# Performance work log

Measured on AMD Instinct MI355X. Metric: run time of the kernel, lower is better.

The kernel has to match this reference:

```python
import jax, jax.numpy as jnp
import numpy as np

NEG_SLOPE = 0.2
LN_EPS = 1e-5
NUM_LAYERS = 4
H = 3            # num heads (both modalities)
C_MOL = 512      # molecule channels (in == out, required by the cat in forward)
C_PROT = 1280    # protein channels
VOCAB = 512 * 9 + 1
G_MOL = 512      # molecule graphs
G_PROT = 32      # protein graphs


def _with_self_loops(src, dst, n):
    loop = jnp.arange(n, dtype=src.dtype)
    return jnp.concatenate([src, loop]), jnp.concatenate([dst, loop])


def gat_conv(x, src, dst, W, a_src, a_dst, bias):
    """PyG GATConv, concat=False (head-mean), add_self_loops=True.
    x: [N, Fin], W: [Fin, H*C], a_src/a_dst: [H, C], bias: [C]."""
    n = x.shape[0]
    h = (x @ W).reshape(n, a_src.shape[0], a_src.shape[1])   # [N,H,C]
    al_s = jnp.sum(h * a_src, axis=-1)                       # [N,H]
    al_d = jnp.sum(h * a_dst, axis=-1)                       # [N,H]
    s, d = _with_self_loops(src, dst, n)
    e = jax.nn.leaky_relu(al_s[s] + al_d[d], NEG_SLOPE)      # [E+N,H]
    m = jax.ops.segment_max(e, d, num_segments=n)            # segment softmax (stable)
    m = jnp.where(jnp.isfinite(m), m, 0.0)
    p = jnp.exp(e - m[d])
    z = jax.ops.segment_sum(p, d, num_segments=n)
    alpha = p / (z[d] + 1e-16)                               # [E+N,H]
    out = jax.ops.segment_sum(h[s] * alpha[:, :, None], d, num_segments=n)  # [N,H,C]
    return out.mean(axis=1) + bias                           # concat=False -> head mean


def layer_norm(x, g, b):
    mu = x.mean(-1, keepdims=True)
    var = ((x - mu) ** 2).mean(-1, keepdims=True)
    return (x - mu) * jax.lax.rsqrt(var + LN_EPS) * g + b


def mean_pool(x, batch, num_graphs):
    s = jax.ops.segment_sum(x, batch, num_segments=num_graphs)
    cnt = jax.ops.segment_sum(jnp.ones((x.shape[0],), x.dtype), batch, num_segments=num_graphs)
    return s / jnp.maximum(cnt, 1.0)[:, None]


def setup_inputs() -> dict:
    key = jax.random.key(0)
    ks = jax.random.split(key, 20)
    n_mol, e_mol = 40000, 80000
    n_prot, e_prot = 8000, 64000
    drug_x = jax.random.randint(ks[0], (n_mol, 9), 0, VOCAB)
    mol_edge_index = jax.random.randint(ks[1], (2, e_mol), 0, n_mol)
    mol_batch = jnp.sort(jax.random.randint(ks[2], (n_mol,), 0, G_MOL))
    prot_x = jax.random.normal(ks[3], (n_prot, C_PROT), jnp.float32)
    prot_edge_index = jax.random.randint(ks[4], (2, e_prot), 0, n_prot)
    prot_batch = jnp.sort(jax.random.randint(ks[5], (n_prot,), 0, G_PROT))
    sc = 0.02
    emb = (jax.random.normal(ks[6], (VOCAB, C_MOL), jnp.float32) * sc).at[0].set(0.0)  # padding_idx=0
    mol_W = jax.random.normal(ks[7], (NUM_LAYERS, C_MOL, H * C_MOL), jnp.float32) * sc
    mol_asrc = jax.random.normal(ks[8], (NUM_LAYERS, H, C_MOL), jnp.float32) * sc
    mol_adst = jax.random.normal(ks[9], (NUM_LAYERS, H, C_MOL), jnp.float32) * sc
    mol_bias = jnp.zeros((NUM_LAYERS, C_MOL), jnp.float32)
    mol_ln_g = jnp.ones((NUM_LAYERS, C_MOL), jnp.float32)
    mol_ln_b = jnp.zeros((NUM_LAYERS, C_MOL), jnp.float32)
    prot_W = jax.random.normal(ks[10], (NUM_LAYERS, C_PROT, H * C_PROT), jnp.float32) * sc
    prot_asrc = jax.random.normal(ks[11], (NUM_LAYERS, H, C_PROT), jnp.float32) * sc
    prot_adst = jax.random.normal(ks[12], (NUM_LAYERS, H, C_PROT), jnp.float32) * sc
    prot_bias = jnp.zeros((NUM_LAYERS, C_PROT), jnp.float32)
    prot_ln_g = jnp.ones((NUM_LAYERS, C_PROT), jnp.float32)
    prot_ln_b = jnp.zeros((NUM_LAYERS, C_PROT), jnp.float32)
    return dict(drug_x=drug_x, mol_edge_index=mol_edge_index, mol_batch=mol_batch,
                prot_x=prot_x, prot_edge_index=prot_edge_index, prot_batch=prot_batch,
                emb=emb, mol_W=mol_W, mol_asrc=mol_asrc, mol_adst=mol_adst,
                mol_bias=mol_bias, mol_ln_g=mol_ln_g, mol_ln_b=mol_ln_b,
                prot_W=prot_W, prot_asrc=prot_asrc, prot_adst=prot_adst,
                prot_bias=prot_bias, prot_ln_g=prot_ln_g, prot_ln_b=prot_ln_b)


def reference(drug_x, mol_edge_index, mol_batch, prot_x, prot_edge_index, prot_batch,
              emb, mol_W, mol_asrc, mol_adst, mol_bias, mol_ln_g, mol_ln_b,
              prot_W, prot_asrc, prot_adst, prot_bias, prot_ln_g, prot_ln_b):
    # dropout layers are identity (eval mode)
    mol_x = emb[drug_x].mean(axis=-2)                       # [N_mol, C_MOL]
    mol_feats = [mean_pool(mol_x, mol_batch, G_MOL)]
    prot_feats = [mean_pool(prot_x, prot_batch, G_PROT)]
    msrc, mdst = mol_edge_index[0], mol_edge_index[1]
    psrc, pdst = prot_edge_index[0], prot_edge_index[1]
    px = prot_x
    for i in range(NUM_LAYERS):
        mol_x = gat_conv(mol_x, msrc, mdst, mol_W[i], mol_asrc[i], mol_adst[i], mol_bias[i])
        mol_x = layer_norm(mol_x, mol_ln_g[i], mol_ln_b[i])
        px = gat_conv(px, psrc, pdst, prot_W[i], prot_asrc[i], prot_adst[i], prot_bias[i])
        px = layer_norm(px, prot_ln_g[i], prot_ln_b[i])
        mol_feats.append(mean_pool(mol_x, mol_batch, G_MOL))
        prot_feats.append(mean_pool(px, prot_batch, G_PROT))
    return jnp.stack(mol_feats, axis=1), jnp.stack(prot_feats, axis=1)  # [G,5,C] each
```

## Files before the change

kernel.cpp:

```cpp
#include <hip/hip_runtime.h>
#include <cstdint>


constexpr int H_HEADS = 3;
constexpr float NEG_SLOPE = 0.2f;
constexpr float LN_EPS = 1e-5f;
constexpr int N_MOL = 40000, E_MOL = 80000, C_MOL = 512, G_MOL = 512;
constexpr int N_PROT = 8000, E_PROT = 64000, C_PROT = 1280, G_PROT = 32;
constexpr int LAYERS = 4;
constexpr int MPAD_MOL = 40064;
constexpr int MPAD_PROT = 8064;

typedef unsigned short u16;
typedef __attribute__((ext_vector_type(8))) short short8v;
typedef __attribute__((ext_vector_type(4))) unsigned short ushort4v;
typedef __attribute__((ext_vector_type(4))) float f32x4;

__device__ __forceinline__ float bf2f(u16 s) {
    union { unsigned u; float f; } v; v.u = ((unsigned)s) << 16; return v.f;
}
__device__ __forceinline__ u16 f2bf(float f) {
    union { float f; unsigned u; } v; v.f = f;
    return (u16)((v.u + 0x7fffu + ((v.u >> 16) & 1u)) >> 16);
}

__device__ __forceinline__ void g2l16(const void* g, void* l) {
    __builtin_amdgcn_global_load_lds((const __attribute__((address_space(1))) void*)g,
                                     (__attribute__((address_space(3))) void*)l, 16, 0, 0);
}


__global__ void set_int_kernel(int* p, int v, int n) {
    int i = blockIdx.x * blockDim.x + threadIdx.x;
    if (i < n) p[i] = v;
}

__global__ void zero_f32_kernel(float* p, int n) {
    int i = blockIdx.x * blockDim.x + threadIdx.x;
    if (i < n) p[i] = 0.f;
}

__global__ void copy_int_kernel(const int* __restrict__ s, int* __restrict__ d, int n) {
    int i = blockIdx.x * blockDim.x + threadIdx.x;
    if (i < n) d[i] = s[i];
}

__global__ void hist_kernel(const int* __restrict__ keys, int n, int* __restrict__ cnt) {
    int i = blockIdx.x * blockDim.x + threadIdx.x;
    if (i < n) atomicAdd(&cnt[keys[i]], 1);
}

__global__ void scan_kernel(const int* __restrict__ in, int* __restrict__ out, int n) {
    __shared__ int sums[1024];
    const int t = threadIdx.x;
    const int chunk = (n + 1023) / 1024;
    const int start = t * chunk;
    const int end = min(start + chunk, n);
    int s = 0;
    for (int i = start; i < end; ++i) s += in[i];
    sums[t] = s;
    __syncthreads();
    if (t == 0) {
        int acc = 0;
        for (int i = 0; i < 1024; ++i) { int v = sums[i]; sums[i] = acc; acc += v; }
        out[n] = acc;
    }
    __syncthreads();
    int acc = sums[t];
    for (int i = start; i < end; ++i) { out[i] = acc; acc += in[i]; }
}

__global__ void fill_self_kernel(int* __restrict__ pos, int* __restrict__ srcl, int n) {
    int i = blockIdx.x * blockDim.x + threadIdx.x;
    if (i < n) { int slot = atomicAdd(&pos[i], 1); srcl[slot] = i; }
}

__global__ void fill_edge_kernel(const int* __restrict__ src, const int* __restrict__ dst, int e,
                                 int* __restrict__ pos, int* __restrict__ srcl) {
    int i = blockIdx.x * blockDim.x + threadIdx.x;
    if (i < e) { int slot = atomicAdd(&pos[dst[i]], 1); srcl[slot] = src[i]; }
}

__global__ void f32_to_bf16(const float* __restrict__ in, u16* __restrict__ out, int n) {
    int i = blockIdx.x * blockDim.x + threadIdx.x;
    if (i < n) out[i] = f2bf(in[i]);
}


__global__ void embed_mean_kernel(const int* __restrict__ drug_x, const float* __restrict__ emb,
                                  u16* __restrict__ out) {
    const int n = blockIdx.x;
    __shared__ int idx[9];
    if (threadIdx.x < 9) idx[threadIdx.x] = drug_x[n * 9 + threadIdx.x];
    __syncthreads();
    const int c = threadIdx.x;
    float s = 0.f;
#pragma unroll
    for (int t = 0; t < 9; ++t) s += emb[(size_t)idx[t] * C_MOL + c];
    out[(size_t)n * C_MOL + c] = f2bf(s * (1.f / 9.f));
}


__global__ __launch_bounds__(256) void transfold(const float* __restrict__ W, u16* __restrict__ Wt,
                                                 const float* __restrict__ asrc,
                                                 const float* __restrict__ adst,
                                                 float* __restrict__ wsrc, float* __restrict__ wdst,
                                                 int CIN, int COUT, size_t headStride, int ldn) {
    __shared__ float t[32][33];
    __shared__ float rs[8][33], rd[8][33];
    const int h = blockIdx.z;
    const int n0 = blockIdx.x * 32, k0 = blockIdx.y * 32;
    const int tx = threadIdx.x & 31, ty = threadIdx.x >> 5;
#pragma unroll
    for (int q = 0; q < 4; ++q)
        t[ty + q * 8][tx] = W[(size_t)(k0 + ty + q * 8) * (H_HEADS * COUT) + h * COUT + n0 + tx];
    __syncthreads();
#pragma unroll
    for (int q = 0; q < 4; ++q)
        Wt[(size_t)h * headStride + (size_t)(n0 + ty + q * 8) * ldn + k0 + tx] =
            f2bf(t[tx][ty + q * 8]);
    float ps = 0.f, pd = 0.f;
    const float* as = asrc + h * COUT + n0;
    const float* ad = adst + h * COUT + n0;
#pragma unroll
    for (int q = 0; q < 4; ++q) {
        const float w = t[tx][ty + q * 8];
        ps += w * as[ty + q * 8];
        pd += w * ad[ty + q * 8];
    }
    rs[ty][tx] = ps;
    rd[ty][tx] = pd;
    __syncthreads();
    if (ty == 0) {
        float s = 0.f, d = 0.f;
#pragma unroll
        for (int j = 0; j < 8; ++j) { s += rs[j][tx]; d += rd[j][tx]; }
        atomicAdd(&wsrc[h * CIN + k0 + tx], s);
        atomicAdd(&wdst[h * CIN + k0 + tx], d);
    }
}


template <int C>
__global__ void attn_logits(const u16* __restrict__ x, const float* __restrict__ wsrc,
                            const float* __restrict__ wdst, float* __restrict__ als,
                            float* __restrict__ ald) {
    constexpr int PER = C / 64;
    const int n = blockIdx.x, lane = threadIdx.x;
    const u16* xr = x + (size_t)n * C + lane * PER;
    float xv[PER];
#pragma unroll
    for (int i = 0; i < PER; i += 4) {
        const ushort4v v = *(const ushort4v*)(xr + i);
        xv[i] = bf2f(v.x); xv[i + 1] = bf2f(v.y); xv[i + 2] = bf2f(v.z); xv[i + 3] = bf2f(v.w);
    }
    for (int h = 0; h < H_HEADS; ++h) {
        const float* ws = wsrc + h * C + lane * PER;
        const float* wd = wdst + h * C + lane * PER;
        float ss = 0.f, sd = 0.f;
#pragma unroll
        for (int i = 0; i < PER; i += 4) {
            const float4 a = *(const float4*)(ws + i);
            const float4 b = *(const float4*)(wd + i);
            ss += xv[i] * a.x + xv[i + 1] * a.y + xv[i + 2] * a.z + xv[i + 3] * a.w;
            sd += xv[i] * b.x + xv[i + 1] * b.y + xv[i + 2] * b.z + xv[i + 3] * b.w;
        }
        for (int o = 32; o; o >>= 1) { ss += __shfl_down(ss, o); sd += __shfl_down(sd, o); }
        if (lane == 0) { als[n * H_HEADS + h] = ss; ald[n * H_HEADS + h] = sd; }
    }
}


__global__ __launch_bounds__(256) void agg_mol_f(const u16* __restrict__ x,
                                                 const float* __restrict__ als,
                                                 const float* __restrict__ ald,
                                                 const int* __restrict__ indptr,
                                                 const int* __restrict__ srcl,
                                                 u16* __restrict__ agg) {
    constexpr int MAXD = 128;
    const int wv = threadIdx.x >> 6, lane = threadIdx.x & 63;
    const int n = blockIdx.x * 4 + wv;
    const int beg = indptr[n], end = indptr[n + 1];
    const int deg = end - beg;
    __shared__ float atab[4][MAXD * 3];
    float m = -1e30f, zi = 0.f;
    if (lane < H_HEADS) {
        const float ad = ald[n * H_HEADS + lane];
        for (int e = beg; e < end; ++e) {
            float v = als[srcl[e] * H_HEADS + lane] + ad;
            v = v >= 0.f ? v : NEG_SLOPE * v;
            m = fmaxf(m, v);
        }
        float z = 0.f;
        for (int e = beg; e < end; ++e) {
            float v = als[srcl[e] * H_HEADS + lane] + ad;
            v = v >= 0.f ? v : NEG_SLOPE * v;
            z += __expf(v - m);
        }
        zi = 1.f / (z + 1e-16f);
    }
    const float m0 = __shfl(m, 0), m1 = __shfl(m, 1), m2 = __shfl(m, 2);
    const float z0 = __shfl(zi, 0), z1 = __shfl(zi, 1), z2 = __shfl(zi, 2);
    const float ad0 = ald[n * H_HEADS + 0], ad1 = ald[n * H_HEADS + 1], ad2 = ald[n * H_HEADS + 2];
    const bool fits = deg <= MAXD;
    if (fits) {
        for (int i = lane; i < deg * 3; i += 64) {
            const int e = i / 3, h = i - e * 3;
            float v = als[srcl[beg + e] * H_HEADS + h] + (h == 0 ? ad0 : (h == 1 ? ad1 : ad2));
            v = v >= 0.f ? v : NEG_SLOPE * v;
            const float mh = h == 0 ? m0 : (h == 1 ? m1 : m2);
            const float zh = h == 0 ? z0 : (h == 1 ? z1 : z2);
            atab[wv][i] = __expf(v - mh) * zh;
        }
    }
    __syncthreads();
    float acc[H_HEADS][8];
#pragma unroll
    for (int h = 0; h < H_HEADS; ++h)
#pragma unroll
        for (int j = 0; j < 8; ++j) acc[h][j] = 0.f;
    for (int e = 0; e < deg; ++e) {
        const int s = srcl[beg + e];
        float a0, a1, a2;
        if (fits) {
            a0 = atab[wv][e * 3 + 0];
            a1 = atab[wv][e * 3 + 1];
            a2 = atab[wv][e * 3 + 2];
        } else {
            float v0 = als[s * H_HEADS + 0] + ad0; v0 = v0 >= 0.f ? v0 : NEG_SLOPE * v0;
            float v1 = als[s * H_HEADS + 1] + ad1; v1 = v1 >= 0.f ? v1 : NEG_SLOPE * v1;
            float v2 = als[s * H_HEADS + 2] + ad2; v2 = v2 >= 0.f ? v2 : NEG_SLOPE * v2;
            a0 = __expf(v0 - m0) * z0;
            a1 = __expf(v1 - m1) * z1;
            a2 = __expf(v2 - m2) * z2;
        }
        const short8v row = *(const short8v*)(x + (size_t)s * C_MOL + lane * 8);
#pragma unroll
        for (int j = 0; j < 8; ++j) {
            const float f = bf2f((u16)row[j]);
            acc[0][j] += a0 * f; acc[1][j] += a1 * f; acc[2][j] += a2 * f;
        }
    }
    u16* o = agg + (size_t)n * (3 * C_MOL) + lane * 8;
#pragma unroll
    for (int h = 0; h < H_HEADS; ++h) {
        short8v r;
#pragma unroll
        for (int j = 0; j < 8; ++j) r[j] = (short)f2bf(acc[h][j]);
        *(short8v*)(o + h * C_MOL) = r;
    }
}


__global__ __launch_bounds__(320) void agg_prot_f(const u16* __restrict__ x,
                                                  const float* __restrict__ als,
                                                  const float* __restrict__ ald,
                                                  const int* __restrict__ indptr,
                                                  const int* __restrict__ srcl,
                                                  u16* __restrict__ agg) {
    constexpr int MAXD = 512;
    const int n = blockIdx.x, tid = threadIdx.x;
    const int beg = indptr[n], end = indptr[n + 1];
    const int deg = end - beg;
    __shared__ float mz[6];
    __shared__ float atab[MAXD * 3];
    if (tid < H_HEADS) {
        const float ad = ald[n * H_HEADS + tid];
        float m = -1e30f;
        for (int e = beg; e < end; ++e) {
            float v = als[srcl[e] * H_HEADS + tid] + ad;
            v = v >= 0.f ? v : NEG_SLOPE * v;
            m = fmaxf(m, v);
        }
        float z = 0.f;
        for (int e = beg; e < end; ++e) {
            float v = als[srcl[e] * H_HEADS + tid] + ad;
            v = v >= 0.f ? v : NEG_SLOPE * v;
            z += __expf(v - m);
        }
        mz[tid] = m;
        mz[3 + tid] = 1.f / (z + 1e-16f);
    }
    __syncthreads();
    const bool fits = deg <= MAXD;
    if (fits) {
        for (int i = tid; i < deg * 3; i += 320) {
            const int e = i / 3, h = i - e * 3;
            float v = als[srcl[beg + e] * H_HEADS + h] + ald[n * H_HEADS + h];
            v = v >= 0.f ? v : NEG_SLOPE * v;
            atab[i] = __expf(v - mz[h]) * mz[3 + h];
        }
    }
    __syncthreads();
    const float m0 = mz[0], m1 = mz[1], m2 = mz[2];
    const float z0 = mz[3], z1 = mz[4], z2 = mz[5];
    const float ad0 = ald[n * H_HEADS + 0], ad1 = ald[n * H_HEADS + 1], ad2 = ald[n * H_HEADS + 2];
    float acc[H_HEADS][4];
#pragma unroll
    for (int h = 0; h < H_HEADS; ++h)
#pragma unroll
        for (int j = 0; j < 4; ++j) acc[h][j] = 0.f;
    for (int e = 0; e < deg; ++e) {
        const int s = srcl[beg + e];
        float a0, a1, a2;
        if (fits) {
            a0 = atab[e * 3 + 0];
            a1 = atab[e * 3 + 1];
            a2 = atab[e * 3 + 2];
        } else {
            float v0 = als[s * H_HEADS + 0] + ad0; v0 = v0 >= 0.f ? v0 : NEG_SLOPE * v0;
            float v1 = als[s * H_HEADS + 1] + ad1; v1 = v1 >= 0.f ? v1 : NEG_SLOPE * v1;
            float v2 = als[s * H_HEADS + 2] + ad2; v2 = v2 >= 0.f ? v2 : NEG_SLOPE * v2;
            a0 = __expf(v0 - m0) * z0;
            a1 = __expf(v1 - m1) * z1;
            a2 = __expf(v2 - m2) * z2;
        }
        const ushort4v v = *(const ushort4v*)(x + (size_t)s * C_PROT + tid * 4);
        const float f0 = bf2f(v.x), f1 = bf2f(v.y), f2 = bf2f(v.z), f3 = bf2f(v.w);
        acc[0][0] += a0 * f0; acc[0][1] += a0 * f1; acc[0][2] += a0 * f2; acc[0][3] += a0 * f3;
        acc[1][0] += a1 * f0; acc[1][1] += a1 * f1; acc[1][2] += a1 * f2; acc[1][3] += a1 * f3;
        acc[2][0] += a2 * f0; acc[2][1] += a2 * f1; acc[2][2] += a2 * f2; acc[2][3] += a2 * f3;
    }
    u16* o = agg + (size_t)n * (3 * C_PROT) + tid * 4;
#pragma unroll
    for (int h = 0; h < H_HEADS; ++h) {
        ushort4v r;
        r.x = f2bf(acc[h][0]); r.y = f2bf(acc[h][1]); r.z = f2bf(acc[h][2]); r.w = f2bf(acc[h][3]);
        *(ushort4v*)(o + h * C_PROT) = r;
    }
}


__global__ __launch_bounds__(256) void gemm128d(
    const u16* __restrict__ A0, const u16* __restrict__ B0, u16* __restrict__ C0,
    int N0, int K0, int nx0, int M0, int g0,
    const u16* __restrict__ A1, const u16* __restrict__ B1, u16* __restrict__ C1,
    int N1, int K1, int nx1, int M1) {
    __shared__ u16 lds[16384];
    const int tid = threadIdx.x;
    const int w = tid >> 6, l = tid & 63;
    const int wr = w >> 1, wc = w & 1;

    const int bid = blockIdx.x;
    const u16 *A, *Bt;
    u16* Cout;
    int N, K, nxch, Mreal, base, sz;
    if (bid < g0) { base = 0; sz = g0; A = A0; Bt = B0; Cout = C0; N = N0; K = K0; nxch = nx0; Mreal = M0; }
    else { base = g0; sz = gridDim.x - g0; A = A1; Bt = B1; Cout = C1; N = N1; K = K1; nxch = nx1; Mreal = M1; }
    const int j = bid - base;
    const int q = sz >> 3, r = sz & 7;
    const int xcd = j & 7, idx = j >> 3;
    const int wg = (xcd < r ? xcd * (q + 1) : r * (q + 1) + (xcd - r) * q) + idx;
    const int nx = wg % nxch, my = wg / nxch;
    const size_t bm = (size_t)my * 128, bn = (size_t)nx * 128;

    const f32x4 zf = {0.f, 0.f, 0.f, 0.f};
    f32x4 acc[4][4];
#pragma unroll
    for (int i = 0; i < 4; ++i)
#pragma unroll
        for (int jj = 0; jj < 4; ++jj) acc[i][jj] = zf;

    const int srow = w * 32 + (l >> 3);
    const int sseg = (l & 7) ^ (l >> 3);
    const u16* Ab = A + (bm + srow) * (size_t)K + sseg * 8;
    const u16* Bb = Bt + (bn + srow) * (size_t)K + sseg * 8;

    for (int k0 = 0; k0 < K; k0 += 64) {
#pragma unroll
        for (int qq = 0; qq < 4; ++qq)
            g2l16(Ab + k0 + (size_t)qq * 8 * K, lds + (w * 4 + qq) * 512);
#pragma unroll
        for (int qq = 0; qq < 4; ++qq)
            g2l16(Bb + k0 + (size_t)qq * 8 * K, lds + 8192 + (w * 4 + qq) * 512);
        __syncthreads();
#pragma unroll
        for (int kk = 0; kk < 2; ++kk) {
            const int sg = ((kk * 4 + (l >> 4)) ^ (l & 7)) * 8;
            short8v af[4], bf8[4];
#pragma unroll
            for (int fm = 0; fm < 4; ++fm) {
                const int row = wr * 64 + fm * 16 + (l & 15);
                af[fm] = *(const short8v*)&lds[row * 64 + sg];
            }
#pragma unroll
            for (int fn = 0; fn < 4; ++fn) {
                const int row = wc * 64 + fn * 16 + (l & 15);
                bf8[fn] = *(const short8v*)&lds[8192 + row * 64 + sg];
            }
#pragma unroll
            for (int fm = 0; fm < 4; ++fm)
#pragma unroll
                for (int fn = 0; fn < 4; ++fn)
                    acc[fm][fn] = __builtin_amdgcn_mfma_f32_16x16x32_bf16(af[fm], bf8[fn],
                                                                          acc[fm][fn], 0, 0, 0);
        }
        __syncthreads();
    }

#pragma unroll
    for (int half = 0; half < 2; ++half) {
        if (wr == half) {
#pragma unroll
            for (int fm = 0; fm < 4; ++fm)
#pragma unroll
                for (int fn = 0; fn < 4; ++fn) {
                    const int col = wc * 64 + fn * 16 + (l & 15);
#pragma unroll
                    for (int rr = 0; rr < 4; ++rr)
                        lds[(fm * 16 + (l >> 4) * 4 + rr) * 136 + col] = f2bf(acc[fm][fn][rr]);
                }
        }
        __syncthreads();
        const int lrow = tid >> 2, lseg = tid & 3;
        const size_t grow = bm + half * 64 + lrow;
        if (grow < (size_t)Mreal) {
            u16* Crow = Cout + grow * (size_t)N + bn + lseg * 32;
            const u16* Lr = lds + lrow * 136 + lseg * 32;
#pragma unroll
            for (int ii = 0; ii < 4; ++ii)
                *(float4*)(Crow + ii * 8) = *(const float4*)(Lr + ii * 8);
        }
        __syncthreads();
    }
}


template <int C, int LOGITS>
__global__ __launch_bounds__(C / 4) void ln_kernel(u16* __restrict__ x,
                                                   const float* __restrict__ bias,
                                                   const float* __restrict__ g,
                                                   const float* __restrict__ b,
                                                   const float* __restrict__ wsrc_n,
                                                   const float* __restrict__ wdst_n,
                                                   float* __restrict__ als,
                                                   float* __restrict__ ald) {
    constexpr int NT = C / 4;
    constexpr int NW = NT / 64;
    const int n = blockIdx.x, tid = threadIdx.x;
    u16* xr = x + (size_t)n * C + tid * 4;
    constexpr float invH = 1.f / (float)H_HEADS;
    const ushort4v xv = *(const ushort4v*)xr;
    const float4 bi = *(const float4*)(bias + tid * 4);
    const float v0 = bf2f(xv.x) * invH + bi.x;
    const float v1 = bf2f(xv.y) * invH + bi.y;
    const float v2 = bf2f(xv.z) * invH + bi.z;
    const float v3 = bf2f(xv.w) * invH + bi.w;
    float s1 = v0 + v1 + v2 + v3;
    float s2 = v0 * v0 + v1 * v1 + v2 * v2 + v3 * v3;
    __shared__ float red[2][NW];
    __shared__ float red2[NW][6];
    for (int o = 32; o; o >>= 1) { s1 += __shfl_down(s1, o); s2 += __shfl_down(s2, o); }
    if ((tid & 63) == 0) { red[0][tid >> 6] = s1; red[1][tid >> 6] = s2; }
    __syncthreads();
    float t1 = 0.f, t2 = 0.f;
#pragma unroll
    for (int i = 0; i < NW; ++i) { t1 += red[0][i]; t2 += red[1][i]; }
    const float mu = t1 / C;
    const float var = t2 / C - mu * mu;
    const float rstd = rsqrtf(var + LN_EPS);
    const float4 gg = *(const float4*)(g + tid * 4);
    const float4 bb = *(const float4*)(b + tid * 4);
    ushort4v ov;
    ov.x = f2bf((v0 - mu) * rstd * gg.x + bb.x);
    ov.y = f2bf((v1 - mu) * rstd * gg.y + bb.y);
    ov.z = f2bf((v2 - mu) * rstd * gg.z + bb.z);
    ov.w = f2bf((v3 - mu) * rstd * gg.w + bb.w);
    *(ushort4v*)xr = ov;
    if (LOGITS) {
        const float q0 = bf2f(ov.x), q1 = bf2f(ov.y), q2 = bf2f(ov.z), q3 = bf2f(ov.w);
        float ps[3], pd[3];
#pragma unroll
        for (int h = 0; h < 3; ++h) {
            const float4 a = *(const float4*)(wsrc_n + h * C + tid * 4);
            const float4 d = *(const float4*)(wdst_n + h * C + tid * 4);
            ps[h] = q0 * a.x + q1 * a.y + q2 * a.z + q3 * a.w;
            pd[h] = q0 * d.x + q1 * d.y + q2 * d.z + q3 * d.w;
        }
        for (int o = 32; o; o >>= 1) {
#pragma unroll
            for (int h = 0; h < 3; ++h) {
                ps[h] += __shfl_down(ps[h], o);
                pd[h] += __shfl_down(pd[h], o);
            }
        }
        if ((tid & 63) == 0) {
            const int wv = tid >> 6;
#pragma unroll
            for (int h = 0; h < 3; ++h) { red2[wv][h] = ps[h]; red2[wv][3 + h] = pd[h]; }
        }
        __syncthreads();
        if (tid == 0) {
#pragma unroll
            for (int h = 0; h < 3; ++h) {
                float as = 0.f, ad = 0.f;
#pragma unroll
                for (int i = 0; i < NW; ++i) { as += red2[i][h]; ad += red2[i][3 + h]; }
                als[n * H_HEADS + h] = as;
                ald[n * H_HEADS + h] = ad;
            }
        }
    }
}


template <int C, int S>
__global__ void pool_atomic(const u16* __restrict__ x, const int* __restrict__ goff,
                            float* __restrict__ out, int layer) {
    const int g = blockIdx.x, seg = blockIdx.y;
    const int beg = goff[g], end = goff[g + 1];
    const int len = end - beg;
    const int s0 = beg + (len * seg) / S;
    const int s1 = beg + (len * (seg + 1)) / S;
    if (s0 >= s1) return;
    const float inv = 1.f / fmaxf((float)len, 1.f);
    const int tid = threadIdx.x;
    float a0 = 0.f, a1 = 0.f, a2 = 0.f, a3 = 0.f;
    for (int n = s0; n < s1; ++n) {
        const ushort4v v = *(const ushort4v*)(x + (size_t)n * C + tid * 4);
        a0 += bf2f(v.x); a1 += bf2f(v.y); a2 += bf2f(v.z); a3 += bf2f(v.w);
    }
    float* o = out + ((size_t)g * (LAYERS + 1) + layer) * C + tid * 4;
    atomicAdd(o + 0, a0 * inv);
    atomicAdd(o + 1, a1 * inv);
    atomicAdd(o + 2, a2 * inv);
    atomicAdd(o + 3, a3 * inv);
}


extern "C" void kernel_launch(void* const* d_in, const int* in_sizes, int n_in, void* d_out,
                              int out_size, void* d_ws, size_t ws_size, hipStream_t stream) {
    const int* drug_x      = (const int*)d_in[0];
    const int* mol_ei      = (const int*)d_in[1];
    const int* mol_batch   = (const int*)d_in[2];
    const float* prot_in   = (const float*)d_in[3];
    const int* prot_ei     = (const int*)d_in[4];
    const int* prot_batch  = (const int*)d_in[5];
    const float* emb       = (const float*)d_in[6];
    const float* mol_W     = (const float*)d_in[7];
    const float* mol_asrc  = (const float*)d_in[8];
    const float* mol_adst  = (const float*)d_in[9];
    const float* mol_bias  = (const float*)d_in[10];
    const float* mol_lng   = (const float*)d_in[11];
    const float* mol_lnb   = (const float*)d_in[12];
    const float* prot_W    = (const float*)d_in[13];
    const float* prot_asrc = (const float*)d_in[14];
    const float* prot_adst = (const float*)d_in[15];
    const float* prot_bias = (const float*)d_in[16];
    const float* prot_lng  = (const float*)d_in[17];
    const float* prot_lnb  = (const float*)d_in[18];

    if (ws_size < (size_t)240500000) return;
    const bool BIG = ws_size >= (size_t)262000000;

    char* base = (char*)d_ws;
    size_t off = 0;
    auto alloc = [&](size_t bytes) -> void* {
        void* r = base + off;
        off = (off + bytes + 255) & ~(size_t)255;
        return r;
    };
    u16* x_mol  = (u16*)alloc((size_t)N_MOL * C_MOL * 2);
    u16* x_prot = (u16*)alloc((size_t)N_PROT * C_PROT * 2);
    u16* aggM   = (u16*)alloc((size_t)3 * MPAD_MOL * C_MOL * 2);
    u16* WtM    = (u16*)alloc((size_t)H_HEADS * C_MOL * C_MOL * 2);
    u16* WtP    = (u16*)alloc((size_t)H_HEADS * C_PROT * C_PROT * 2);
    u16* aggP   = BIG ? (u16*)alloc((size_t)3 * MPAD_PROT * C_PROT * 2) : aggM;
    float* wsrcM = (float*)alloc((size_t)LAYERS * H_HEADS * C_MOL * 4);
    float* wdstM = (float*)alloc((size_t)LAYERS * H_HEADS * C_MOL * 4);
    float* wsrcP = (float*)alloc((size_t)LAYERS * H_HEADS * C_PROT * 4);
    float* wdstP = (float*)alloc((size_t)LAYERS * H_HEADS * C_PROT * 4);
    float* alsM = (float*)alloc((size_t)N_MOL * H_HEADS * 4);
    float* aldM = (float*)alloc((size_t)N_MOL * H_HEADS * 4);
    float* alsP = (float*)alloc((size_t)N_PROT * H_HEADS * 4);
    float* aldP = (float*)alloc((size_t)N_PROT * H_HEADS * 4);
    int* mol_indptr  = (int*)alloc((N_MOL + 1) * 4);
    int* mol_pos     = (int*)alloc(N_MOL * 4);
    int* mol_srcl    = (int*)alloc((E_MOL + N_MOL) * 4);
    int* prot_indptr = (int*)alloc((N_PROT + 1) * 4);
    int* prot_pos    = (int*)alloc(N_PROT * 4);
    int* prot_srcl   = (int*)alloc((E_PROT + N_PROT) * 4);
    int* cnt         = (int*)alloc(N_MOL * 4);
    int* mol_goff    = (int*)alloc((G_MOL + 1) * 4);
    int* prot_goff   = (int*)alloc((G_PROT + 1) * 4);
    int* gcnt        = (int*)alloc(G_MOL * 4);

    float* out_mol  = (float*)d_out;
    float* out_prot = (float*)d_out + (size_t)G_MOL * (LAYERS + 1) * C_MOL;

    zero_f32_kernel<<<(out_size + 255) / 256, 256, 0, stream>>>((float*)d_out, out_size);
    zero_f32_kernel<<<(LAYERS * H_HEADS * C_MOL + 255) / 256, 256, 0, stream>>>(
        wsrcM, LAYERS * H_HEADS * C_MOL);
    zero_f32_kernel<<<(LAYERS * H_HEADS * C_MOL + 255) / 256, 256, 0, stream>>>(
        wdstM, LAYERS * H_HEADS * C_MOL);
    zero_f32_kernel<<<(LAYERS * H_HEADS * C_PROT + 255) / 256, 256, 0, stream>>>(
        wsrcP, LAYERS * H_HEADS * C_PROT);
    zero_f32_kernel<<<(LAYERS * H_HEADS * C_PROT + 255) / 256, 256, 0, stream>>>(
        wdstP, LAYERS * H_HEADS * C_PROT);

    set_int_kernel<<<(N_MOL + 255) / 256, 256, 0, stream>>>(cnt, 1, N_MOL);
    hist_kernel<<<(E_MOL + 255) / 256, 256, 0, stream>>>(mol_ei + E_MOL, E_MOL, cnt);
    scan_kernel<<<1, 1024, 0, stream>>>(cnt, mol_indptr, N_MOL);
    copy_int_kernel<<<(N_MOL + 255) / 256, 256, 0, stream>>>(mol_indptr, mol_pos, N_MOL);
    fill_self_kernel<<<(N_MOL + 255) / 256, 256, 0, stream>>>(mol_pos, mol_srcl, N_MOL);
    fill_edge_kernel<<<(E_MOL + 255) / 256, 256, 0, stream>>>(mol_ei, mol_ei + E_MOL, E_MOL, mol_pos,
                                                              mol_srcl);
    set_int_kernel<<<(N_PROT + 255) / 256, 256, 0, stream>>>(cnt, 1, N_PROT);
    hist_kernel<<<(E_PROT + 255) / 256, 256, 0, stream>>>(prot_ei + E_PROT, E_PROT, cnt);
    scan_kernel<<<1, 1024, 0, stream>>>(cnt, prot_indptr, N_PROT);
    copy_int_kernel<<<(N_PROT + 255) / 256, 256, 0, stream>>>(prot_indptr, prot_pos, N_PROT);
    fill_self_kernel<<<(N_PROT + 255) / 256, 256, 0, stream>>>(prot_pos, prot_srcl, N_PROT);
    fill_edge_kernel<<<(E_PROT + 255) / 256, 256, 0, stream>>>(prot_ei, prot_ei + E_PROT, E_PROT,
                                                               prot_pos, prot_srcl);

    set_int_kernel<<<(G_MOL + 255) / 256, 256, 0, stream>>>(gcnt, 0, G_MOL);
    hist_kernel<<<(N_MOL + 255) / 256, 256, 0, stream>>>(mol_batch, N_MOL, gcnt);
    scan_kernel<<<1, 1024, 0, stream>>>(gcnt, mol_goff, G_MOL);
    set_int_kernel<<<(G_PROT + 255) / 256, 256, 0, stream>>>(gcnt, 0, G_PROT);
    hist_kernel<<<(N_PROT + 255) / 256, 256, 0, stream>>>(prot_batch, N_PROT, gcnt);
    scan_kernel<<<1, 1024, 0, stream>>>(gcnt, prot_goff, G_PROT);

    transfold<<<dim3(C_MOL / 32, C_MOL / 32, H_HEADS), 256, 0, stream>>>(
        mol_W, WtM, mol_asrc, mol_adst, wsrcM, wdstM, C_MOL, C_MOL, (size_t)C_MOL, 3 * C_MOL);
    transfold<<<dim3(C_PROT / 32, C_PROT / 32, H_HEADS), 256, 0, stream>>>(
        prot_W, WtP, prot_asrc, prot_adst, wsrcP, wdstP, C_PROT, C_PROT, (size_t)C_PROT,
        3 * C_PROT);

    f32_to_bf16<<<(N_PROT * C_PROT + 255) / 256, 256, 0, stream>>>(prot_in, x_prot, N_PROT * C_PROT);
    embed_mean_kernel<<<N_MOL, C_MOL, 0, stream>>>(drug_x, emb, x_mol);
    pool_atomic<C_MOL, 8><<<dim3(G_MOL, 8), C_MOL / 4, 0, stream>>>(x_mol, mol_goff, out_mol, 0);
    pool_atomic<C_PROT, 64><<<dim3(G_PROT, 64), C_PROT / 4, 0, stream>>>(x_prot, prot_goff,
                                                                         out_prot, 0);
    attn_logits<C_MOL><<<N_MOL, 64, 0, stream>>>(x_mol, wsrcM, wdstM, alsM, aldM);
    attn_logits<C_PROT><<<N_PROT, 64, 0, stream>>>(x_prot, wsrcP, wdstP, alsP, aldP);

    const int gMol = (MPAD_MOL / 128) * (C_MOL / 128);
    const int gProt = (MPAD_PROT / 128) * (C_PROT / 128);

    for (int l = 0; l < LAYERS; ++l) {
        const int last = (l == LAYERS - 1);
        if (BIG) {
            agg_mol_f<<<N_MOL / 4, 256, 0, stream>>>(x_mol, alsM, aldM, mol_indptr, mol_srcl, aggM);
            agg_prot_f<<<N_PROT, 320, 0, stream>>>(x_prot, alsP, aldP, prot_indptr, prot_srcl,
                                                   aggP);
            gemm128d<<<gProt + gMol, 256, 0, stream>>>(
                aggP, WtP, x_prot, C_PROT, 3 * C_PROT, C_PROT / 128, N_PROT, gProt,
                aggM, WtM, x_mol, C_MOL, 3 * C_MOL, C_MOL / 128, N_MOL);
            if (!last) {
                transfold<<<dim3(C_MOL / 32, C_MOL / 32, H_HEADS), 256, 0, stream>>>(
                    mol_W + (size_t)(l + 1) * C_MOL * (H_HEADS * C_MOL), WtM,
                    mol_asrc + (size_t)(l + 1) * H_HEADS * C_MOL,
                    mol_adst + (size_t)(l + 1) * H_HEADS * C_MOL,
                    wsrcM + (size_t)(l + 1) * H_HEADS * C_MOL,
                    wdstM + (size_t)(l + 1) * H_HEADS * C_MOL, C_MOL, C_MOL, (size_t)C_MOL,
                    3 * C_MOL);
                transfold<<<dim3(C_PROT / 32, C_PROT / 32, H_HEADS), 256, 0, stream>>>(
                    prot_W + (size_t)(l + 1) * C_PROT * (H_HEADS * C_PROT), WtP,
                    prot_asrc + (size_t)(l + 1) * H_HEADS * C_PROT,
                    prot_adst + (size_t)(l + 1) * H_HEADS * C_PROT,
                    wsrcP + (size_t)(l + 1) * H_HEADS * C_PROT,
                    wdstP + (size_t)(l + 1) * H_HEADS * C_PROT, C_PROT, C_PROT, (size_t)C_PROT,
                    3 * C_PROT);
                ln_kernel<C_MOL, 1><<<N_MOL, C_MOL / 4, 0, stream>>>(
                    x_mol, mol_bias + (size_t)l * C_MOL, mol_lng + (size_t)l * C_MOL,
                    mol_lnb + (size_t)l * C_MOL, wsrcM + (size_t)(l + 1) * H_HEADS * C_MOL,
                    wdstM + (size_t)(l + 1) * H_HEADS * C_MOL, alsM, aldM);
                ln_kernel<C_PROT, 1><<<N_PROT, C_PROT / 4, 0, stream>>>(
                    x_prot, prot_bias + (size_t)l * C_PROT, prot_lng + (size_t)l * C_PROT,
                    prot_lnb + (size_t)l * C_PROT, wsrcP + (size_t)(l + 1) * H_HEADS * C_PROT,
                    wdstP + (size_t)(l + 1) * H_HEADS * C_PROT, alsP, aldP);
            } else {
                ln_kernel<C_MOL, 0><<<N_MOL, C_MOL / 4, 0, stream>>>(
                    x_mol, mol_bias + (size_t)l * C_MOL, mol_lng + (size_t)l * C_MOL,
                    mol_lnb + (size_t)l * C_MOL, nullptr, nullptr, nullptr, nullptr);
                ln_kernel<C_PROT, 0><<<N_PROT, C_PROT / 4, 0, stream>>>(
                    x_prot, prot_bias + (size_t)l * C_PROT, prot_lng + (size_t)l * C_PROT,
                    prot_lnb + (size_t)l * C_PROT, nullptr, nullptr, nullptr, nullptr);
            }
            pool_atomic<C_MOL, 8><<<dim3(G_MOL, 8), C_MOL / 4, 0, stream>>>(x_mol, mol_goff,
                                                                            out_mol, l + 1);
            pool_atomic<C_PROT, 64><<<dim3(G_PROT, 64), C_PROT / 4, 0, stream>>>(
                x_prot, prot_goff, out_prot, l + 1);
        } else {
            agg_mol_f<<<N_MOL / 4, 256, 0, stream>>>(x_mol, alsM, aldM, mol_indptr, mol_srcl, aggM);
            gemm128d<<<gMol, 256, 0, stream>>>(
                aggM, WtM, x_mol, C_MOL, 3 * C_MOL, C_MOL / 128, N_MOL, gMol,
                aggM, WtM, x_mol, C_MOL, 3 * C_MOL, C_MOL / 128, N_MOL);
            if (!last)
                transfold<<<dim3(C_MOL / 32, C_MOL / 32, H_HEADS), 256, 0, stream>>>(
                    mol_W + (size_t)(l + 1) * C_MOL * (H_HEADS * C_MOL), WtM,
                    mol_asrc + (size_t)(l + 1) * H_HEADS * C_MOL,
                    mol_adst + (size_t)(l + 1) * H_HEADS * C_MOL,
                    wsrcM + (size_t)(l + 1) * H_HEADS * C_MOL,
                    wdstM + (size_t)(l + 1) * H_HEADS * C_MOL, C_MOL, C_MOL, (size_t)C_MOL,
                    3 * C_MOL);
            if (last)
                ln_kernel<C_MOL, 0><<<N_MOL, C_MOL / 4, 0, stream>>>(
                    x_mol, mol_bias + (size_t)l * C_MOL, mol_lng + (size_t)l * C_MOL,
                    mol_lnb + (size_t)l * C_MOL, nullptr, nullptr, nullptr, nullptr);
            else
                ln_kernel<C_MOL, 1><<<N_MOL, C_MOL / 4, 0, stream>>>(
                    x_mol, mol_bias + (size_t)l * C_MOL, mol_lng + (size_t)l * C_MOL,
                    mol_lnb + (size_t)l * C_MOL, wsrcM + (size_t)(l + 1) * H_HEADS * C_MOL,
                    wdstM + (size_t)(l + 1) * H_HEADS * C_MOL, alsM, aldM);
            pool_atomic<C_MOL, 8><<<dim3(G_MOL, 8), C_MOL / 4, 0, stream>>>(x_mol, mol_goff,
                                                                            out_mol, l + 1);
            agg_prot_f<<<N_PROT, 320, 0, stream>>>(x_prot, alsP, aldP, prot_indptr, prot_srcl,
                                                   aggP);
            gemm128d<<<gProt, 256, 0, stream>>>(
                aggP, WtP, x_prot, C_PROT, 3 * C_PROT, C_PROT / 128, N_PROT, gProt,
                aggP, WtP, x_prot, C_PROT, 3 * C_PROT, C_PROT / 128, N_PROT);
            if (!last)
                transfold<<<dim3(C_PROT / 32, C_PROT / 32, H_HEADS), 256, 0, stream>>>(
                    prot_W + (size_t)(l + 1) * C_PROT * (H_HEADS * C_PROT), WtP,
                    prot_asrc + (size_t)(l + 1) * H_HEADS * C_PROT,
                    prot_adst + (size_t)(l + 1) * H_HEADS * C_PROT,
                    wsrcP + (size_t)(l + 1) * H_HEADS * C_PROT,
                    wdstP + (size_t)(l + 1) * H_HEADS * C_PROT, C_PROT, C_PROT, (size_t)C_PROT,
                    3 * C_PROT);
            if (last)
                ln_kernel<C_PROT, 0><<<N_PROT, C_PROT / 4, 0, stream>>>(
                    x_prot, prot_bias + (size_t)l * C_PROT, prot_lng + (size_t)l * C_PROT,
                    prot_lnb + (size_t)l * C_PROT, nullptr, nullptr, nullptr, nullptr);
            else
                ln_kernel<C_PROT, 1><<<N_PROT, C_PROT / 4, 0, stream>>>(
                    x_prot, prot_bias + (size_t)l * C_PROT, prot_lng + (size_t)l * C_PROT,
                    prot_lnb + (size_t)l * C_PROT, wsrcP + (size_t)(l + 1) * H_HEADS * C_PROT,
                    wdstP + (size_t)(l + 1) * H_HEADS * C_PROT, alsP, aldP);
            pool_atomic<C_PROT, 64><<<dim3(G_PROT, 64), C_PROT / 4, 0, stream>>>(
                x_prot, prot_goff, out_prot, l + 1);
        }
    }
}
```

Baseline: 2.271 ms.

## Merge mol/prot aggregation into one launch and fuse mean-pool into layernorm

Combines the molecule and protein attention-aggregation kernels into a single launch: each 320-thread block handles either 5 molecule nodes (one per wave) or one protein node, with a shared smem buffer. It also folds the per-graph mean pooling into the layernorm kernel through atomic adds into the output, removing the separate pool kernels. The small-workspace fallback path is dropped, so the kernel now always needs the larger workspace, and the protein MAXD drops to 500 so its table fits the shared buffer. Per-node atomics add contention on the pooled outputs compared with the previous chunked pooling.

```diff
diff --git a/kernel.cpp b/kernel.cpp
--- a/kernel.cpp
+++ b/kernel.cpp
@@ -171,18 +171,18 @@
 }
 
 
-__global__ __launch_bounds__(256) void agg_mol_f(const u16* __restrict__ x,
-                                                 const float* __restrict__ als,
-                                                 const float* __restrict__ ald,
-                                                 const int* __restrict__ indptr,
-                                                 const int* __restrict__ srcl,
-                                                 u16* __restrict__ agg) {
+__device__ __forceinline__ void agg_mol_part(const u16* __restrict__ x,
+                                             const float* __restrict__ als,
+                                             const float* __restrict__ ald,
+                                             const int* __restrict__ indptr,
+                                             const int* __restrict__ srcl, u16* __restrict__ agg,
+                                             float* smem) {
     constexpr int MAXD = 128;
     const int wv = threadIdx.x >> 6, lane = threadIdx.x & 63;
-    const int n = blockIdx.x * 4 + wv;
+    const int n = blockIdx.x * 5 + wv;
     const int beg = indptr[n], end = indptr[n + 1];
     const int deg = end - beg;
-    __shared__ float atab[4][MAXD * 3];
+    float* atab = smem + wv * (MAXD * 3);
     float m = -1e30f, zi = 0.f;
     if (lane < H_HEADS) {
         const float ad = ald[n * H_HEADS + lane];
@@ -210,7 +210,7 @@
             v = v >= 0.f ? v : NEG_SLOPE * v;
             const float mh = h == 0 ? m0 : (h == 1 ? m1 : m2);
             const float zh = h == 0 ? z0 : (h == 1 ? z1 : z2);
-            atab[wv][i] = __expf(v - mh) * zh;
+            atab[i] = __expf(v - mh) * zh;
         }
     }
     __syncthreads();
@@ -223,16 +223,12 @@
         const int s = srcl[beg + e];
         float a0, a1, a2;
         if (fits) {
-            a0 = atab[wv][e * 3 + 0];
-            a1 = atab[wv][e * 3 + 1];
-            a2 = atab[wv][e * 3 + 2];
+            a0 = atab[e * 3 + 0]; a1 = atab[e * 3 + 1]; a2 = atab[e * 3 + 2];
         } else {
             float v0 = als[s * H_HEADS + 0] + ad0; v0 = v0 >= 0.f ? v0 : NEG_SLOPE * v0;
             float v1 = als[s * H_HEADS + 1] + ad1; v1 = v1 >= 0.f ? v1 : NEG_SLOPE * v1;
             float v2 = als[s * H_HEADS + 2] + ad2; v2 = v2 >= 0.f ? v2 : NEG_SLOPE * v2;
-            a0 = __expf(v0 - m0) * z0;
-            a1 = __expf(v1 - m1) * z1;
-            a2 = __expf(v2 - m2) * z2;
+            a0 = __expf(v0 - m0) * z0; a1 = __expf(v1 - m1) * z1; a2 = __expf(v2 - m2) * z2;
         }
         const short8v row = *(const short8v*)(x + (size_t)s * C_MOL + lane * 8);
 #pragma unroll
@@ -251,19 +247,18 @@
     }
 }
 
-
-__global__ __launch_bounds__(320) void agg_prot_f(const u16* __restrict__ x,
-                                                  const float* __restrict__ als,
-                                                  const float* __restrict__ ald,
-                                                  const int* __restrict__ indptr,
-                                                  const int* __restrict__ srcl,
-                                                  u16* __restrict__ agg) {
-    constexpr int MAXD = 512;
-    const int n = blockIdx.x, tid = threadIdx.x;
+__device__ __forceinline__ void agg_prot_part(const u16* __restrict__ x,
+                                              const float* __restrict__ als,
+                                              const float* __restrict__ ald,
+                                              const int* __restrict__ indptr,
+                                              const int* __restrict__ srcl, u16* __restrict__ agg,
+                                              float* smem, int n) {
+    constexpr int MAXD = 500;
+    const int tid = threadIdx.x;
     const int beg = indptr[n], end = indptr[n + 1];
     const int deg = end - beg;
-    __shared__ float mz[6];
-    __shared__ float atab[MAXD * 3];
+    float* mz = smem;
+    float* atab = smem + 6;
     if (tid < H_HEADS) {
         const float ad = ald[n * H_HEADS + tid];
         float m = -1e30f;
@@ -304,16 +299,12 @@
         const int s = srcl[beg + e];
         float a0, a1, a2;
         if (fits) {
-            a0 = atab[e * 3 + 0];
-            a1 = atab[e * 3 + 1];
-            a2 = atab[e * 3 + 2];
+            a0 = atab[e * 3 + 0]; a1 = atab[e * 3 + 1]; a2 = atab[e * 3 + 2];
         } else {
             float v0 = als[s * H_HEADS + 0] + ad0; v0 = v0 >= 0.f ? v0 : NEG_SLOPE * v0;
             float v1 = als[s * H_HEADS + 1] + ad1; v1 = v1 >= 0.f ? v1 : NEG_SLOPE * v1;
             float v2 = als[s * H_HEADS + 2] + ad2; v2 = v2 >= 0.f ? v2 : NEG_SLOPE * v2;
-            a0 = __expf(v0 - m0) * z0;
-            a1 = __expf(v1 - m1) * z1;
-            a2 = __expf(v2 - m2) * z2;
+            a0 = __expf(v0 - m0) * z0; a1 = __expf(v1 - m1) * z1; a2 = __expf(v2 - m2) * z2;
         }
         const ushort4v v = *(const ushort4v*)(x + (size_t)s * C_PROT + tid * 4);
         const float f0 = bf2f(v.x), f1 = bf2f(v.y), f2 = bf2f(v.z), f3 = bf2f(v.w);
@@ -328,6 +319,19 @@
         r.x = f2bf(acc[h][0]); r.y = f2bf(acc[h][1]); r.z = f2bf(acc[h][2]); r.w = f2bf(acc[h][3]);
         *(ushort4v*)(o + h * C_PROT) = r;
     }
+}
+
+__global__ __launch_bounds__(320) void agg_both(
+    const u16* __restrict__ xM, const float* __restrict__ alsM, const float* __restrict__ aldM,
+    const int* __restrict__ iptrM, const int* __restrict__ srclM, u16* __restrict__ aggM,
+    const u16* __restrict__ xP, const float* __restrict__ alsP, const float* __restrict__ aldP,
+    const int* __restrict__ iptrP, const int* __restrict__ srclP, u16* __restrict__ aggP,
+    int molBlocks) {
+    __shared__ float smem[1920];
+    if ((int)blockIdx.x < molBlocks)
+        agg_mol_part(xM, alsM, aldM, iptrM, srclM, aggM, smem);
+    else
+        agg_prot_part(xP, alsP, aldP, iptrP, srclP, aggP, smem, blockIdx.x - molBlocks);
 }
 
 
@@ -427,14 +431,17 @@
 
 
 template <int C, int LOGITS>
-__global__ __launch_bounds__(C / 4) void ln_kernel(u16* __restrict__ x,
-                                                   const float* __restrict__ bias,
-                                                   const float* __restrict__ g,
-                                                   const float* __restrict__ b,
-                                                   const float* __restrict__ wsrc_n,
-                                                   const float* __restrict__ wdst_n,
-                                                   float* __restrict__ als,
-                                                   float* __restrict__ ald) {
+__global__ __launch_bounds__(C / 4) void ln_pool(u16* __restrict__ x,
+                                                 const float* __restrict__ bias,
+                                                 const float* __restrict__ g,
+                                                 const float* __restrict__ b,
+                                                 const int* __restrict__ batch,
+                                                 const int* __restrict__ goff,
+                                                 float* __restrict__ out, int layer,
+                                                 const float* __restrict__ wsrc_n,
+                                                 const float* __restrict__ wdst_n,
+                                                 float* __restrict__ als,
+                                                 float* __restrict__ ald) {
     constexpr int NT = C / 4;
     constexpr int NW = NT / 64;
     const int n = blockIdx.x, tid = threadIdx.x;
@@ -467,8 +474,17 @@
     ov.z = f2bf((v2 - mu) * rstd * gg.z + bb.z);
     ov.w = f2bf((v3 - mu) * rstd * gg.w + bb.w);
     *(ushort4v*)xr = ov;
+    const float q0 = bf2f(ov.x), q1 = bf2f(ov.y), q2 = bf2f(ov.z), q3 = bf2f(ov.w);
+    {
+        const int gr = batch[n];
+        const float inv = 1.f / fmaxf((float)(goff[gr + 1] - goff[gr]), 1.f);
+        float* o = out + ((size_t)gr * (LAYERS + 1) + layer) * C + tid * 4;
+        atomicAdd(o + 0, q0 * inv);
+        atomicAdd(o + 1, q1 * inv);
+        atomicAdd(o + 2, q2 * inv);
+        atomicAdd(o + 3, q3 * inv);
+    }
     if (LOGITS) {
-        const float q0 = bf2f(ov.x), q1 = bf2f(ov.y), q2 = bf2f(ov.z), q3 = bf2f(ov.w);
         float ps[3], pd[3];
 #pragma unroll
         for (int h = 0; h < 3; ++h) {
@@ -550,8 +566,7 @@
     const float* prot_lng  = (const float*)d_in[17];
     const float* prot_lnb  = (const float*)d_in[18];
 
-    if (ws_size < (size_t)240500000) return;
-    const bool BIG = ws_size >= (size_t)262000000;
+    if (ws_size < (size_t)262000000) return;
 
     char* base = (char*)d_ws;
     size_t off = 0;
@@ -565,7 +580,7 @@
     u16* aggM   = (u16*)alloc((size_t)3 * MPAD_MOL * C_MOL * 2);
     u16* WtM    = (u16*)alloc((size_t)H_HEADS * C_MOL * C_MOL * 2);
     u16* WtP    = (u16*)alloc((size_t)H_HEADS * C_PROT * C_PROT * 2);
-    u16* aggP   = BIG ? (u16*)alloc((size_t)3 * MPAD_PROT * C_PROT * 2) : aggM;
+    u16* aggP   = (u16*)alloc((size_t)3 * MPAD_PROT * C_PROT * 2);
     float* wsrcM = (float*)alloc((size_t)LAYERS * H_HEADS * C_MOL * 4);
     float* wdstM = (float*)alloc((size_t)LAYERS * H_HEADS * C_MOL * 4);
     float* wsrcP = (float*)alloc((size_t)LAYERS * H_HEADS * C_PROT * 4);
@@ -636,99 +651,50 @@
 
     const int gMol = (MPAD_MOL / 128) * (C_MOL / 128);
     const int gProt = (MPAD_PROT / 128) * (C_PROT / 128);
+    const int molAggBlocks = N_MOL / 5;
 
     for (int l = 0; l < LAYERS; ++l) {
         const int last = (l == LAYERS - 1);
-        if (BIG) {
-            agg_mol_f<<<N_MOL / 4, 256, 0, stream>>>(x_mol, alsM, aldM, mol_indptr, mol_srcl, aggM);
-            agg_prot_f<<<N_PROT, 320, 0, stream>>>(x_prot, alsP, aldP, prot_indptr, prot_srcl,
-                                                   aggP);
-            gemm128d<<<gProt + gMol, 256, 0, stream>>>(
-                aggP, WtP, x_prot, C_PROT, 3 * C_PROT, C_PROT / 128, N_PROT, gProt,
-                aggM, WtM, x_mol, C_MOL, 3 * C_MOL, C_MOL / 128, N_MOL);
-            if (!last) {
-                transfold<<<dim3(C_MOL / 32, C_MOL / 32, H_HEADS), 256, 0, stream>>>(
-                    mol_W + (size_t)(l + 1) * C_MOL * (H_HEADS * C_MOL), WtM,
-                    mol_asrc + (size_t)(l + 1) * H_HEADS * C_MOL,
-                    mol_adst + (size_t)(l + 1) * H_HEADS * C_MOL,
-                    wsrcM + (size_t)(l + 1) * H_HEADS * C_MOL,
-                    wdstM + (size_t)(l + 1) * H_HEADS * C_MOL, C_MOL, C_MOL, (size_t)C_MOL,
-                    3 * C_MOL);
-                transfold<<<dim3(C_PROT / 32, C_PROT / 32, H_HEADS), 256, 0, stream>>>(
-                    prot_W + (size_t)(l + 1) * C_PROT * (H_HEADS * C_PROT), WtP,
-                    prot_asrc + (size_t)(l + 1) * H_HEADS * C_PROT,
-                    prot_adst + (size_t)(l + 1) * H_HEADS * C_PROT,
-                    wsrcP + (size_t)(l + 1) * H_HEADS * C_PROT,
-                    wdstP + (size_t)(l + 1) * H_HEADS * C_PROT, C_PROT, C_PROT, (size_t)C_PROT,
-                    3 * C_PROT);
-                ln_kernel<C_MOL, 1><<<N_MOL, C_MOL / 4, 0, stream>>>(
-                    x_mol, mol_bias + (size_t)l * C_MOL, mol_lng + (size_t)l * C_MOL,
-                    mol_lnb + (size_t)l * C_MOL, wsrcM + (size_t)(l + 1) * H_HEADS * C_MOL,
-                    wdstM + (size_t)(l + 1) * H_HEADS * C_MOL, alsM, aldM);
-                ln_kernel<C_PROT, 1><<<N_PROT, C_PROT / 4, 0, stream>>>(
-                    x_prot, prot_bias + (size_t)l * C_PROT, prot_lng + (size_t)l * C_PROT,
-                    prot_lnb + (size_t)l * C_PROT, wsrcP + (size_t)(l + 1) * H_HEADS * C_PROT,
-                    wdstP + (size_t)(l + 1) * H_HEADS * C_PROT, alsP, aldP);
-            } else {
-                ln_kernel<C_MOL, 0><<<N_MOL, C_MOL / 4, 0, stream>>>(
-                    x_mol, mol_bias + (size_t)l * C_MOL, mol_lng + (size_t)l * C_MOL,
-                    mol_lnb + (size_t)l * C_MOL, nullptr, nullptr, nullptr, nullptr);
-                ln_kernel<C_PROT, 0><<<N_PROT, C_PROT / 4, 0, stream>>>(
-                    x_prot, prot_bias + (size_t)l * C_PROT, prot_lng + (size_t)l * C_PROT,
-                    prot_lnb + (size_t)l * C_PROT, nullptr, nullptr, nullptr, nullptr);
-            }
-            pool_atomic<C_MOL, 8><<<dim3(G_MOL, 8), C_MOL / 4, 0, stream>>>(x_mol, mol_goff,
-                                                                            out_mol, l + 1);
-            pool_atomic<C_PROT, 64><<<dim3(G_PROT, 64), C_PROT / 4, 0, stream>>>(
-                x_prot, prot_goff, out_prot, l + 1);
+        agg_both<<<molAggBlocks + N_PROT, 320, 0, stream>>>(
+            x_mol, alsM, aldM, mol_indptr, mol_srcl, aggM,
+            x_prot, alsP, aldP, prot_indptr, prot_srcl, aggP, molAggBlocks);
+        gemm128d<<<gProt + gMol, 256, 0, stream>>>(
+            aggP, WtP, x_prot, C_PROT, 3 * C_PROT, C_PROT / 128, N_PROT, gProt,
+            aggM, WtM, x_mol, C_MOL, 3 * C_MOL, C_MOL / 128, N_MOL);
+        if (!last) {
+            transfold<<<dim3(C_MOL / 32, C_MOL / 32, H_HEADS), 256, 0, stream>>>(
+                mol_W + (size_t)(l + 1) * C_MOL * (H_HEADS * C_MOL), WtM,
+                mol_asrc + (size_t)(l + 1) * H_HEADS * C_MOL,
+                mol_adst + (size_t)(l + 1) * H_HEADS * C_MOL,
+                wsrcM + (size_t)(l + 1) * H_HEADS * C_MOL,
+                wdstM + (size_t)(l + 1) * H_HEADS * C_MOL, C_MOL, C_MOL, (size_t)C_MOL,
+                3 * C_MOL);
+            transfold<<<dim3(C_PROT / 32, C_PROT / 32, H_HEADS), 256, 0, stream>>>(
+                prot_W + (size_t)(l + 1) * C_PROT * (H_HEADS * C_PROT), WtP,
+                prot_asrc + (size_t)(l + 1) * H_HEADS * C_PROT,
+                prot_adst + (size_t)(l + 1) * H_HEADS * C_PROT,
+                wsrcP + (size_t)(l + 1) * H_HEADS * C_PROT,
+                wdstP + (size_t)(l + 1) * H_HEADS * C_PROT, C_PROT, C_PROT, (size_t)C_PROT,
+                3 * C_PROT);
+            ln_pool<C_MOL, 1><<<N_MOL, C_MOL / 4, 0, stream>>>(
+                x_mol, mol_bias + (size_t)l * C_MOL, mol_lng + (size_t)l * C_MOL,
+                mol_lnb + (size_t)l * C_MOL, mol_batch, mol_goff, out_mol, l + 1,
+                wsrcM + (size_t)(l + 1) * H_HEADS * C_MOL,
+                wdstM + (size_t)(l + 1) * H_HEADS * C_MOL, alsM, aldM);
+            ln_pool<C_PROT, 1><<<N_PROT, C_PROT / 4, 0, stream>>>(
+                x_prot, prot_bias + (size_t)l * C_PROT, prot_lng + (size_t)l * C_PROT,
+                prot_lnb + (size_t)l * C_PROT, prot_batch, prot_goff, out_prot, l + 1,
+                wsrcP + (size_t)(l + 1) * H_HEADS * C_PROT,
+                wdstP + (size_t)(l + 1) * H_HEADS * C_PROT, alsP, aldP);
         } else {
-            agg_mol_f<<<N_MOL / 4, 256, 0, stream>>>(x_mol, alsM, aldM, mol_indptr, mol_srcl, aggM);
-            gemm128d<<<gMol, 256, 0, stream>>>(
-                aggM, WtM, x_mol, C_MOL, 3 * C_MOL, C_MOL / 128, N_MOL, gMol,
-                aggM, WtM, x_mol, C_MOL, 3 * C_MOL, C_MOL / 128, N_MOL);
-            if (!last)
-                transfold<<<dim3(C_MOL / 32, C_MOL / 32, H_HEADS), 256, 0, stream>>>(
-                    mol_W + (size_t)(l + 1) * C_MOL * (H_HEADS * C_MOL), WtM,
-                    mol_asrc + (size_t)(l + 1) * H_HEADS * C_MOL,
-                    mol_adst + (size_t)(l + 1) * H_HEADS * C_MOL,
-                    wsrcM + (size_t)(l + 1) * H_HEADS * C_MOL,
-                    wdstM + (size_t)(l + 1) * H_HEADS * C_MOL, C_MOL, C_MOL, (size_t)C_MOL,
-                    3 * C_MOL);
-            if (last)
-                ln_kernel<C_MOL, 0><<<N_MOL, C_MOL / 4, 0, stream>>>(
-                    x_mol, mol_bias + (size_t)l * C_MOL, mol_lng + (size_t)l * C_MOL,
-                    mol_lnb + (size_t)l * C_MOL, nullptr, nullptr, nullptr, nullptr);
-            else
-                ln_kernel<C_MOL, 1><<<N_MOL, C_MOL / 4, 0, stream>>>(
-                    x_mol, mol_bias + (size_t)l * C_MOL, mol_lng + (size_t)l * C_MOL,
-                    mol_lnb + (size_t)l * C_MOL, wsrcM + (size_t)(l + 1) * H_HEADS * C_MOL,
-                    wdstM + (size_t)(l + 1) * H_HEADS * C_MOL, alsM, aldM);
-            pool_atomic<C_MOL, 8><<<dim3(G_MOL, 8), C_MOL / 4, 0, stream>>>(x_mol, mol_goff,
-                                                                            out_mol, l + 1);
-            agg_prot_f<<<N_PROT, 320, 0, stream>>>(x_prot, alsP, aldP, prot_indptr, prot_srcl,
-                                                   aggP);
-            gemm128d<<<gProt, 256, 0, stream>>>(
-                aggP, WtP, x_prot, C_PROT, 3 * C_PROT, C_PROT / 128, N_PROT, gProt,
-                aggP, WtP, x_prot, C_PROT, 3 * C_PROT, C_PROT / 128, N_PROT);
-            if (!last)
-                transfold<<<dim3(C_PROT / 32, C_PROT / 32, H_HEADS), 256, 0, stream>>>(
-                    prot_W + (size_t)(l + 1) * C_PROT * (H_HEADS * C_PROT), WtP,
-                    prot_asrc + (size_t)(l + 1) * H_HEADS * C_PROT,
-                    prot_adst + (size_t)(l + 1) * H_HEADS * C_PROT,
-                    wsrcP + (size_t)(l + 1) * H_HEADS * C_PROT,
-                    wdstP + (size_t)(l + 1) * H_HEADS * C_PROT, C_PROT, C_PROT, (size_t)C_PROT,
-                    3 * C_PROT);
-            if (last)
-                ln_kernel<C_PROT, 0><<<N_PROT, C_PROT / 4, 0, stream>>>(
-                    x_prot, prot_bias + (size_t)l * C_PROT, prot_lng + (size_t)l * C_PROT,
-                    prot_lnb + (size_t)l * C_PROT, nullptr, nullptr, nullptr, nullptr);
-            else
-                ln_kernel<C_PROT, 1><<<N_PROT, C_PROT / 4, 0, stream>>>(
-                    x_prot, prot_bias + (size_t)l * C_PROT, prot_lng + (size_t)l * C_PROT,
-                    prot_lnb + (size_t)l * C_PROT, wsrcP + (size_t)(l + 1) * H_HEADS * C_PROT,
-                    wdstP + (size_t)(l + 1) * H_HEADS * C_PROT, alsP, aldP);
-            pool_atomic<C_PROT, 64><<<dim3(G_PROT, 64), C_PROT / 4, 0, stream>>>(
-                x_prot, prot_goff, out_prot, l + 1);
-        }
-    }
-}
+            ln_pool<C_MOL, 0><<<N_MOL, C_MOL / 4, 0, stream>>>(
+                x_mol, mol_bias + (size_t)l * C_MOL, mol_lng + (size_t)l * C_MOL,
+                mol_lnb + (size_t)l * C_MOL, mol_batch, mol_goff, out_mol, l + 1, nullptr,
+                nullptr, nullptr, nullptr);
+            ln_pool<C_PROT, 0><<<N_PROT, C_PROT / 4, 0, stream>>>(
+                x_prot, prot_bias + (size_t)l * C_PROT, prot_lng + (size_t)l * C_PROT,
+                prot_lnb + (size_t)l * C_PROT, prot_batch, prot_goff, out_prot, l + 1, nullptr,
+                nullptr, nullptr, nullptr);
+        }
+    }
+}
```

New measurement: 3.820 ms. 68.2% more time.
